# Optimization experiments

Measured on AMD Instinct MI355X. Metric: run time of the kernel, lower is better.

## Reference

```python
import jax, jax.numpy as jnp
import numpy as np

UNITS = 256

def _lstm_step(carry, idx, kernel, rec_kernel, bias, num_chars):
    h, c = carry
    x = jax.nn.one_hot(idx, num_chars, dtype=h.dtype)          # [B, num_chars]
    z = x @ kernel + h @ rec_kernel + bias                      # [B, 4*UNITS]
    i, f, g, o = jnp.split(z, 4, axis=-1)                       # Keras gate order i,f,c,o
    i = jax.nn.sigmoid(i)
    f = jax.nn.sigmoid(f)
    g = jnp.tanh(g)
    o = jax.nn.sigmoid(o)
    c_new = f * c + i * g
    h_new = o * jnp.tanh(c_new)
    return (h_new, c_new), None


def setup_inputs() -> dict:
    key = jax.random.key(0)
    ks = jax.random.split(key, 4)
    num_chars, batch, seq_len = 128, 1024, 512
    x = jax.random.randint(ks[0], (batch, seq_len), 0, num_chars, dtype=jnp.int32)
    kernel = jax.random.normal(ks[1], (num_chars, 4 * UNITS), dtype=jnp.float32) * 0.05
    rec_kernel = jax.random.normal(ks[2], (UNITS, 4 * UNITS), dtype=jnp.float32) * 0.05
    bias = jnp.zeros((4 * UNITS,), dtype=jnp.float32)
    dense_w = jax.random.normal(ks[3], (UNITS, num_chars), dtype=jnp.float32) * 0.05
    dense_b = jnp.zeros((num_chars,), dtype=jnp.float32)
    return {"x": x, "kernel": kernel, "rec_kernel": rec_kernel, "bias": bias,
            "dense_w": dense_w, "dense_b": dense_b}


def reference(x, kernel, rec_kernel, bias, dense_w, dense_b):
    batch = x.shape[0]
    num_chars = kernel.shape[0]
    h0 = jnp.zeros((batch, UNITS), dtype=kernel.dtype)
    c0 = jnp.zeros((batch, UNITS), dtype=kernel.dtype)
    step = lambda carry, idx: _lstm_step(carry, idx, kernel, rec_kernel, bias, num_chars)
    (h, _), _ = jax.lax.scan(step, (h0, c0), x.T)  # scan over time: [S, B]
    logits = h @ dense_w + dense_b                  # [B, num_chars]
    return jax.nn.softmax(logits, axis=-1)
```

## Files before the change

kernel.cpp:

```cpp
#include <hip/hip_runtime.h>
#include <cstdint>

typedef __bf16 bf16x8 __attribute__((ext_vector_type(8)));
typedef float  f32x4  __attribute__((ext_vector_type(4)));

union U4B { uint4 u; bf16x8 b; };
__device__ __forceinline__ bf16x8 as_bf(uint4 u) { U4B x; x.u = u; return x.b; }

__device__ __forceinline__ unsigned short f2b(float x) {
  unsigned int u = __float_as_uint(x);
  unsigned int r = (u + 0x7fffu + ((u >> 16) & 1u)) >> 16;
  return (unsigned short)r;
}
__device__ __forceinline__ float b2f(unsigned int bits_lo16) {
  return __uint_as_float(bits_lo16 << 16);
}

__device__ __forceinline__ float sigm(float x) {
  float e = __builtin_amdgcn_exp2f(x * -1.4426950408889634f);
  return __builtin_amdgcn_rcpf(1.0f + e);
}
__device__ __forceinline__ float tanh_fast(float x) {
  float e = __builtin_amdgcn_exp2f(x * 2.8853900817779268f);
  return 1.0f - 2.0f * __builtin_amdgcn_rcpf(e + 1.0f);
}

__global__ void prep_kernel(const float* __restrict__ rec,
                            const float* __restrict__ kern,
                            const float* __restrict__ bias,
                            const float* __restrict__ dw,
                            unsigned short* __restrict__ recT,
                            unsigned short* __restrict__ kb2,
                            unsigned short* __restrict__ dwT) {
  int id = blockIdx.x * 256 + threadIdx.x;
  if (id < 262144) {
    int colp = id >> 8, k = id & 255;
    int u = colp >> 2, g = colp & 3;
    recT[colp * 256 + k] = f2b(rec[k * 1024 + u + 256 * g]);
  } else if (id < 262144 + 131072) {
    int i = id - 262144;
    int ch = i >> 10, colp = i & 1023;
    int u = colp >> 2, g = colp & 3;
    int oc = u + 256 * g;
    kb2[ch * 1024 + colp] = f2b(kern[ch * 1024 + oc] + bias[oc]);
  } else {
    int i = id - 262144 - 131072;
    int cls = i >> 8, k = i & 255;
    dwT[cls * 256 + k] = f2b(dw[k * 128 + cls]);
  }
}

__global__ __launch_bounds__(1024, 4) void lstm_kernel(
    const unsigned short* __restrict__ recT,
    const unsigned short* __restrict__ kb2,
    const unsigned short* __restrict__ dwT,
    const int* __restrict__ x,
    const float* __restrict__ dense_b,
    float* __restrict__ out) {
  __shared__ unsigned short h_buf[2][16][264];
  __shared__ int   x_lds[16][516];
  __shared__ float l_lds[16][132];

  const int tid   = threadIdx.x;
  const int lane  = tid & 63;
  const int wid   = tid >> 6;
  const int row16 = lane & 15;
  const int kg    = lane >> 4;
  const int rbase = blockIdx.x << 4;

  for (int e = tid; e < 16 * 512; e += 1024) {
    int r = e >> 9, c = e & 511;
    x_lds[r][c] = x[(rbase + r) * 512 + c];
  }
  for (int e = tid; e < 16 * 264; e += 1024) (&h_buf[0][0][0])[e] = 0;

  const unsigned short* recBase = recT + ((wid * 64 + row16) * 256 + kg * 8);
  uint4 af[4][8];
#pragma unroll
  for (int m = 0; m < 4; ++m)
#pragma unroll
    for (int k = 0; k < 8; ++k)
      af[m][k] = *(const uint4*)(recBase + m * 16 * 256 + k * 32);

  float c_state[4];
#pragma unroll
  for (int m = 0; m < 4; ++m) c_state[m] = 0.0f;

  __syncthreads();

  for (int t = 0; t < 512; ++t) {
    const int cur = t & 1, nxt = cur ^ 1;

    int idx = x_lds[row16][t];
    const unsigned short* kbBase = kb2 + (idx * 1024 + wid * 64 + kg * 4);
    uint2 kq[4];
#pragma unroll
    for (int m = 0; m < 4; ++m) kq[m] = *(const uint2*)(kbBase + m * 16);

    uint4 hf[8];
#pragma unroll
    for (int k = 0; k < 8; ++k)
      hf[k] = *(const uint4*)&h_buf[cur][row16][k * 32 + kg * 8];

    f32x4 acc[4];
#pragma unroll
    for (int m = 0; m < 4; ++m) {
      f32x4 a = {0.f, 0.f, 0.f, 0.f};
#pragma unroll
      for (int k = 0; k < 8; ++k)
        a = __builtin_amdgcn_mfma_f32_16x16x32_bf16(as_bf(af[m][k]), as_bf(hf[k]), a, 0, 0, 0);
      acc[m] = a;
    }

#pragma unroll
    for (int m = 0; m < 4; ++m) {
      float zi = acc[m][0] + b2f(kq[m].x & 0xffffu);
      float zf = acc[m][1] + b2f(kq[m].x >> 16);
      float zg = acc[m][2] + b2f(kq[m].y & 0xffffu);
      float zo = acc[m][3] + b2f(kq[m].y >> 16);
      float gi = sigm(zi);
      float gf = sigm(zf);
      float gg = tanh_fast(zg);
      float go = sigm(zo);
      float c  = gf * c_state[m] + gi * gg;
      c_state[m] = c;
      float h  = go * tanh_fast(c);
      h_buf[nxt][row16][wid * 16 + m * 4 + kg] = f2b(h);
    }
    __syncthreads();
  }

  if (wid < 8) {
    const unsigned short* dwBase = dwT + ((wid * 16 + row16) * 256 + kg * 8);
    uint4 hf[8];
#pragma unroll
    for (int k = 0; k < 8; ++k)
      hf[k] = *(const uint4*)&h_buf[0][row16][k * 32 + kg * 8];
    f32x4 la = {0.f, 0.f, 0.f, 0.f};
#pragma unroll
    for (int k = 0; k < 8; ++k) {
      uint4 afd = *(const uint4*)(dwBase + k * 32);
      la = __builtin_amdgcn_mfma_f32_16x16x32_bf16(as_bf(afd), as_bf(hf[k]), la, 0, 0, 0);
    }
#pragma unroll
    for (int r = 0; r < 4; ++r) {
      int cls = wid * 16 + kg * 4 + r;
      l_lds[row16][cls] = la[r] + dense_b[cls];
    }
  }
  __syncthreads();

  if (tid < 512) {
    int r = tid >> 5, cg = tid & 31;
    float4 v = *(const float4*)&l_lds[r][cg * 4];
    float mx = fmaxf(fmaxf(v.x, v.y), fmaxf(v.z, v.w));
#pragma unroll
    for (int s = 1; s < 32; s <<= 1) mx = fmaxf(mx, __shfl_xor(mx, s));
    const float L2E = 1.4426950408889634f;
    float e0 = __builtin_amdgcn_exp2f((v.x - mx) * L2E);
    float e1 = __builtin_amdgcn_exp2f((v.y - mx) * L2E);
    float e2 = __builtin_amdgcn_exp2f((v.z - mx) * L2E);
    float e3 = __builtin_amdgcn_exp2f((v.w - mx) * L2E);
    float sm = e0 + e1 + e2 + e3;
#pragma unroll
    for (int s = 1; s < 32; s <<= 1) sm += __shfl_xor(sm, s);
    float inv = __builtin_amdgcn_rcpf(sm);
    float4 o = {e0 * inv, e1 * inv, e2 * inv, e3 * inv};
    *(float4*)&out[(rbase + r) * 128 + cg * 4] = o;
  }
}

extern "C" void kernel_launch(void* const* d_in, const int* in_sizes, int n_in,
                              void* d_out, int out_size, void* d_ws, size_t ws_size,
                              hipStream_t stream) {
  const int*   x      = (const int*)d_in[0];
  const float* kern   = (const float*)d_in[1];
  const float* rec    = (const float*)d_in[2];
  const float* bias   = (const float*)d_in[3];
  const float* dw     = (const float*)d_in[4];
  const float* db     = (const float*)d_in[5];
  float* outp = (float*)d_out;

  unsigned char* ws = (unsigned char*)d_ws;
  unsigned short* recT = (unsigned short*)(ws);
  unsigned short* kb2  = (unsigned short*)(ws + 524288);
  unsigned short* dwT  = (unsigned short*)(ws + 786432);

  prep_kernel<<<1664, 256, 0, stream>>>(rec, kern, bias, dw, recT, kb2, dwT);
  lstm_kernel<<<64, 1024, 0, stream>>>(recT, kb2, dwT, x, db, outp);
}
```

Measured before the change: 3.154 ms.

## Split recurrent weights across registers, LDS, and streamed global loads

```diff
diff --git a/kernel.cpp b/kernel.cpp
--- a/kernel.cpp
+++ b/kernel.cpp
@@ -57,9 +57,8 @@
     const int* __restrict__ x,
     const float* __restrict__ dense_b,
     float* __restrict__ out) {
-  __shared__ unsigned short h_buf[2][16][264];
-  __shared__ int   x_lds[16][516];
-  __shared__ float l_lds[16][132];
+  __shared__ uint4 A_lds[16][8][64];
+  __shared__ unsigned short h_buf[2][16][296];
 
   const int tid   = threadIdx.x;
   const int lane  = tid & 63;
@@ -68,50 +67,78 @@
   const int kg    = lane >> 4;
   const int rbase = blockIdx.x << 4;
 
-  for (int e = tid; e < 16 * 512; e += 1024) {
-    int r = e >> 9, c = e & 511;
-    x_lds[r][c] = x[(rbase + r) * 512 + c];
-  }
-  for (int e = tid; e < 16 * 264; e += 1024) (&h_buf[0][0][0])[e] = 0;
-
   const unsigned short* recBase = recT + ((wid * 64 + row16) * 256 + kg * 8);
-  uint4 af[4][8];
-#pragma unroll
-  for (int m = 0; m < 4; ++m)
-#pragma unroll
-    for (int k = 0; k < 8; ++k)
-      af[m][k] = *(const uint4*)(recBase + m * 16 * 256 + k * 32);
+
+  uint4 af[8];
+#pragma unroll
+  for (int k = 0; k < 8; ++k) {
+    af[k] = *(const uint4*)(recBase + k * 32);
+    asm volatile("" : "+v"(af[k].x), "+v"(af[k].y), "+v"(af[k].z), "+v"(af[k].w));
+  }
+
+#pragma unroll
+  for (int k = 0; k < 8; ++k)
+    A_lds[wid][k][lane] = *(const uint4*)(recBase + 4096 + k * 32);
+
+  const unsigned short* sb2 = recBase + 2 * 4096;
+  const unsigned short* sb3 = recBase + 3 * 4096;
+  uint4 st2[4], st3[4];
+#pragma unroll
+  for (int k = 0; k < 4; ++k) {
+    st2[k] = *(const uint4*)(sb2 + k * 32);
+    st3[k] = *(const uint4*)(sb3 + k * 32);
+  }
+
+  for (int e = tid; e < 2 * 16 * 296; e += 1024) (&h_buf[0][0][0])[e] = 0;
 
   float c_state[4];
 #pragma unroll
   for (int m = 0; m < 4; ++m) c_state[m] = 0.0f;
 
+  const int* xrow = x + (rbase + row16) * 512;
+  int idx_cur = xrow[0];
+
   __syncthreads();
 
+  int cur = 0;
+  const unsigned aoff_base = (unsigned)(((wid * 8) * 64 + lane) * 16);
+
+#pragma unroll 1
   for (int t = 0; t < 512; ++t) {
-    const int cur = t & 1, nxt = cur ^ 1;
-
-    int idx = x_lds[row16][t];
-    const unsigned short* kbBase = kb2 + (idx * 1024 + wid * 64 + kg * 4);
+    unsigned z6 = 0, zL = 0;
+    asm volatile("" : "+v"(z6), "+v"(zL));
+    const unsigned short* sb2v = sb2 + z6;
+    const unsigned short* sb3v = sb3 + z6;
+    const unsigned aoff = aoff_base + zL;
+
+    int idx_next = xrow[(t + 1 < 512) ? t + 1 : 511];
+
+    const unsigned short* hrow = &h_buf[cur][row16][0];
+    const unsigned short* kb = kb2 + (idx_cur * 1024 + wid * 64 + kg * 4);
     uint2 kq[4];
-#pragma unroll
-    for (int m = 0; m < 4; ++m) kq[m] = *(const uint2*)(kbBase + m * 16);
-
-    uint4 hf[8];
-#pragma unroll
-    for (int k = 0; k < 8; ++k)
-      hf[k] = *(const uint4*)&h_buf[cur][row16][k * 32 + kg * 8];
 
     f32x4 acc[4];
 #pragma unroll
-    for (int m = 0; m < 4; ++m) {
-      f32x4 a = {0.f, 0.f, 0.f, 0.f};
-#pragma unroll
-      for (int k = 0; k < 8; ++k)
-        a = __builtin_amdgcn_mfma_f32_16x16x32_bf16(as_bf(af[m][k]), as_bf(hf[k]), a, 0, 0, 0);
-      acc[m] = a;
-    }
-
+    for (int m = 0; m < 4; ++m) acc[m] = f32x4{0.f, 0.f, 0.f, 0.f};
+
+#pragma unroll
+    for (int k = 0; k < 8; ++k) {
+      uint4 hf = *(const uint4*)(hrow + k * 32 + kg * 8);
+      acc[0] = __builtin_amdgcn_mfma_f32_16x16x32_bf16(as_bf(af[k]), as_bf(hf), acc[0], 0, 0, 0);
+      uint4 a1 = *(const uint4*)((const char*)A_lds + k * 1024 + aoff);
+      acc[1] = __builtin_amdgcn_mfma_f32_16x16x32_bf16(as_bf(a1), as_bf(hf), acc[1], 0, 0, 0);
+      acc[2] = __builtin_amdgcn_mfma_f32_16x16x32_bf16(as_bf(st2[k & 3]), as_bf(hf), acc[2], 0, 0, 0);
+      acc[3] = __builtin_amdgcn_mfma_f32_16x16x32_bf16(as_bf(st3[k & 3]), as_bf(hf), acc[3], 0, 0, 0);
+      const int kp = (k + 4) & 7;
+      st2[k & 3] = *(const uint4*)(sb2v + kp * 32);
+      st3[k & 3] = *(const uint4*)(sb3v + kp * 32);
+      if (k == 4) {
+#pragma unroll
+        for (int m = 0; m < 4; ++m) kq[m] = *(const uint2*)(kb + m * 16);
+      }
+    }
+
+    unsigned short* hn = &h_buf[cur ^ 1][row16][wid * 16 + kg];
 #pragma unroll
     for (int m = 0; m < 4; ++m) {
       float zi = acc[m][0] + b2f(kq[m].x & 0xffffu);
@@ -125,11 +152,14 @@
       float c  = gf * c_state[m] + gi * gg;
       c_state[m] = c;
       float h  = go * tanh_fast(c);
-      h_buf[nxt][row16][wid * 16 + m * 4 + kg] = f2b(h);
+      hn[m * 4] = f2b(h);
     }
     __syncthreads();
-  }
-
+    cur ^= 1;
+    idx_cur = idx_next;
+  }
+
+  float (*l_lds)[132] = (float (*)[132])A_lds;
   if (wid < 8) {
     const unsigned short* dwBase = dwT + ((wid * 16 + row16) * 256 + kg * 8);
     uint4 hf[8];
```

New measurement: 4.674 ms. 48.2% more time.
